# Performance work log

Hardware: AMD Instinct MI355X
Metric: run time of the kernel (lower is better)

The kernel has to match this reference:

```python
import jax, jax.numpy as jnp
import numpy as np

B, T = 64, 64
HUMAN, IN = 64, 8
HS, ES, K = 1024, 1024, 7
PSI_H, PSI_LR = 1024, 30

_PAR_SHAPES = [(HS, HS), (HS,), (IN, HS), (HS, HUMAN), (IN, HUMAN - IN)]
_PAR_SIZES = [int(np.prod(s)) for s in _PAR_SHAPES]
N_PSI = int(sum(_PAR_SIZES))
_OFFS = np.cumsum([0] + _PAR_SIZES)


def setup_inputs() -> dict:
    key = jax.random.key(0)
    ks = jax.random.split(key, 16)
    def xav(k, shape):
        lim = float(np.sqrt(6.0 / (shape[0] + shape[1])))
        return jax.random.uniform(k, shape, minval=-lim, maxval=lim, dtype=jnp.float32)
    def uni(k, shape, s):
        return jax.random.uniform(k, shape, minval=-s, maxval=s, dtype=jnp.float32)
    se = float(1.0 / np.sqrt(ES))
    return {
        "inputs": jax.random.normal(ks[0], (B, T, IN), jnp.float32),
        "outputs": jax.random.normal(ks[1], (B, T, HUMAN), jnp.float32),
        "eps": jax.random.normal(ks[2], (B, K), jnp.float32),
        "enc_Wih": uni(ks[3], (3 * ES, HUMAN), se),
        "enc_Whh": uni(ks[4], (3 * ES, ES), se),
        "enc_bih": uni(ks[5], (3 * ES,), se),
        "enc_bhh": uni(ks[6], (3 * ES,), se),
        "to_mu": xav(ks[7], (ES, K)),
        "to_lsigma": xav(ks[8], (ES, K)),
        "to_lsigma_bias": -0.5 * jnp.ones((K,), jnp.float32),
        "W1": xav(ks[9], (K, PSI_H)),
        "b1": jnp.zeros((PSI_H,), jnp.float32),
        "W2": xav(ks[10], (PSI_H, PSI_LR)),
        "b2": jnp.zeros((PSI_LR,), jnp.float32),
        "W3": xav(ks[11], (PSI_LR, N_PSI)),
        "b3": jnp.zeros((N_PSI,), jnp.float32),
        "gru_Wih": xav(ks[12], (IN, 2 * HS)),
        "gru_Whh": xav(ks[13], (HS, 2 * HS)),
        "gru_bias": jnp.concatenate([jnp.zeros((HS,)), jnp.ones((HS,))]).astype(jnp.float32),
    }


def _gru_cell(h, x, Wih, Whh, bih, bhh):
    # torch.nn.GRUCell math, gate order (r, z, n)
    gx = x @ Wih.T + bih
    gh = h @ Whh.T + bhh
    xr, xz, xn = jnp.split(gx, 3, axis=-1)
    hr, hz, hn = jnp.split(gh, 3, axis=-1)
    r = jax.nn.sigmoid(xr + hr)
    z = jax.nn.sigmoid(xz + hz)
    n = jnp.tanh(xn + r * hn)
    return (1.0 - z) * n + z * h


def _split_psi(psi):
    # psi: [B, N_PSI] -> per-sample (Whh, bh, Wih, C, D)
    return [psi[:, _OFFS[i]:_OFFS[i + 1]].reshape((-1,) + _PAR_SHAPES[i]) for i in range(5)]


def reference(inputs, outputs, eps, enc_Wih, enc_Whh, enc_bih, enc_bhh,
              to_mu, to_lsigma, to_lsigma_bias, W1, b1, W2, b2, W3, b3,
              gru_Wih, gru_Whh, gru_bias):
    bsz = inputs.shape[0]
    # ---- encoder: GRUCell over time-major outputs ----
    out_tm = jnp.swapaxes(outputs, 0, 1)  # [T, B, HUMAN]
    h0 = jnp.zeros((bsz, ES), inputs.dtype)
    h_enc = _gru_cell(h0, out_tm[0], enc_Wih, enc_Whh, enc_bih, enc_bhh)
    def enc_step(h, x):
        h = _gru_cell(h, x, enc_Wih, enc_Whh, enc_bih, enc_bhh)
        return h, None
    h_enc, _ = jax.lax.scan(enc_step, h_enc, out_tm[1:])
    mu = h_enc @ to_mu                       # [B, K]
    logstd = h_enc @ to_lsigma + to_lsigma_bias
    z = mu + eps * jnp.exp(logstd)
    # ---- hypernetwork psi decoder ----
    psi = (jnp.tanh(z @ W1 + b1) @ W2 + b2) @ W3 + b3   # [B, N_PSI]
    Whh_b, bh_b, Wih_b, C_b, D_b = _split_psi(psi)
    # ---- per-sample GRU decoder, vectorized over batch, scan over time ----
    gx_all = jnp.einsum('bti,ij->tbj', inputs, gru_Wih)  # [T, B, 2*HS]
    xW_all = jnp.einsum('bti,bih->tbh', inputs, Wih_b)   # [T, B, HS]

    def dec_step(h, xs):
        gx_t, xW_t = xs
        pre = gx_t + h @ gru_Whh + gru_bias   # [B, 2*HS]
        z_t = jax.nn.sigmoid(pre[:, :HS])
        r_t = jax.nn.sigmoid(pre[:, HS:])
        hWhh = jnp.einsum('bh,bhk->bk', h, Whh_b) + bh_b
        eta = jnp.tanh(xW_t + r_t * jnp.tanh(hWhh))
        h_new = z_t * h + (1.0 - z_t) * eta
        return h_new, h_new

    state0 = jnp.zeros((bsz, HS), inputs.dtype)
    h_last, dec_seq = jax.lax.scan(dec_step, state0, (gx_all, xW_all))
    dec_seq = jnp.swapaxes(dec_seq, 0, 1)    # [B, T, HS]
    # ---- readout ----
    yhats = jnp.einsum('bth,bhm->btm', dec_seq, C_b)
    xD = jnp.einsum('bti,bim->btm', inputs, D_b)  # [B, T, HUMAN-IN]
    yhats = yhats + jnp.concatenate([jnp.zeros_like(inputs), xD], axis=-1)
    # residual output
    yhats = yhats + jnp.concatenate(
        [inputs, jnp.zeros((bsz, inputs.shape[1], HUMAN - IN), inputs.dtype)], axis=-1)
    states = jax.lax.stop_gradient(h_last)
    return yhats, mu, logstd, states
```

## Files before the change

kernel.cpp:

```cpp
#include <hip/hip_runtime.h>

namespace {
constexpr int nT = 64;
constexpr int nK = 7;
constexpr long N_PSI = 1123776;
constexpr long SZ_WHH = 1048576;
constexpr long REST_SZ = 75200;
constexpr long R_BH = 0;
constexpr long R_WIH = 1024;
constexpr long R_C = 9216;
constexpr long R_D = 74752;
constexpr int NCH = 16;
constexpr int CHR = 64;
constexpr long PHALF = (long)NCH * 64 * 1024;
}

typedef __attribute__((ext_vector_type(4))) unsigned short us4;

__device__ __forceinline__ float b2f(unsigned short u) {
  return __uint_as_float(((unsigned int)u) << 16);
}
__device__ __forceinline__ unsigned short f2b(float f) {
  unsigned int u = __float_as_uint(f);
  return (unsigned short)((u + 0x7fffu + ((u >> 16) & 1u)) >> 16);
}
__device__ __forceinline__ float sigm(float x) { return 1.f / (1.f + __expf(-x)); }

__global__ void transpose_bf16_k(const float* __restrict__ in, unsigned short* __restrict__ out,
                                 int rows, int cols) {
  __shared__ float tile[32][33];
  int x = blockIdx.x * 32 + threadIdx.x;
  int y = blockIdx.y * 32 + threadIdx.y;
  #pragma unroll
  for (int i = 0; i < 32; i += 8)
    if ((y + i) < rows && x < cols) tile[threadIdx.y + i][threadIdx.x] = in[(long)(y + i) * cols + x];
  __syncthreads();
  x = blockIdx.y * 32 + threadIdx.x;
  y = blockIdx.x * 32 + threadIdx.y;
  #pragma unroll
  for (int i = 0; i < 32; i += 8)
    if ((y + i) < cols && x < rows) out[(long)(y + i) * rows + x] = f2b(tile[threadIdx.x][threadIdx.y + i]);
}

__global__ void cvt_bf16_k(const float* __restrict__ in, unsigned short* __restrict__ out, long n) {
  long i = (long)blockIdx.x * 256 + threadIdx.x;
  if (i < n) out[i] = f2b(in[i]);
}

__global__ __launch_bounds__(256) void enc_gx_k(const float* __restrict__ outputs,
                                                const unsigned short* __restrict__ WtWihB,
                                                const float* __restrict__ bih,
                                                unsigned short* __restrict__ gxE) {
  int g0 = blockIdx.x * 256;
  int btg = blockIdx.y;
  __shared__ unsigned short ws[64 * 256];
  __shared__ float xs[64][64];
  for (int i = threadIdx.x; i < 64 * 256; i += 256)
    ws[i] = WtWihB[(long)(i >> 8) * 3072 + g0 + (i & 255)];
  for (int i = threadIdx.x; i < 64 * 64; i += 256) {
    int idx = btg * 64 + (i >> 6);
    int t = idx >> 6, b = idx & 63;
    xs[i >> 6][i & 63] = outputs[((long)b * nT + t) * 64 + (i & 63)];
  }
  __syncthreads();
  float bihv = bih[g0 + threadIdx.x];
  for (int j = 0; j < 64; ++j) {
    int idx = btg * 64 + j;
    float acc = bihv;
    #pragma unroll 8
    for (int i = 0; i < 64; ++i) acc += xs[j][i] * b2f(ws[i * 256 + threadIdx.x]);
    gxE[(long)idx * 3072 + g0 + threadIdx.x] = f2b(acc);
  }
}

__global__ __launch_bounds__(256) void dec_gx_k(const float* __restrict__ inputs,
                                                const float* __restrict__ gWih,
                                                const float* __restrict__ gbias,
                                                unsigned short* __restrict__ gxD) {
  int g0 = blockIdx.x * 256;
  int btg = blockIdx.y;
  __shared__ float ws[8][256];
  __shared__ float xs[64][8];
  for (int i = threadIdx.x; i < 8 * 256; i += 256)
    ws[i >> 8][i & 255] = gWih[(long)(i >> 8) * 2048 + g0 + (i & 255)];
  for (int i = threadIdx.x; i < 64 * 8; i += 256) {
    int idx = btg * 64 + (i >> 3);
    int t = idx >> 6, b = idx & 63;
    xs[i >> 3][i & 7] = inputs[((long)b * nT + t) * 8 + (i & 7)];
  }
  __syncthreads();
  float bv = gbias[g0 + threadIdx.x];
  for (int j = 0; j < 64; ++j) {
    int idx = btg * 64 + j;
    float acc = bv;
    #pragma unroll
    for (int i = 0; i < 8; ++i) acc += xs[j][i] * ws[i][threadIdx.x];
    gxD[(long)idx * 2048 + g0 + threadIdx.x] = f2b(acc);
  }
}

__global__ __launch_bounds__(256) void xW_k(const float* __restrict__ inputs,
                                            const float* __restrict__ Rest,
                                            unsigned short* __restrict__ xWb) {
  int k0 = blockIdx.x * 256;
  int b = blockIdx.y;
  __shared__ float ws[8][256];
  __shared__ float xs[64][8];
  const float* RB = Rest + (long)b * REST_SZ + R_WIH;
  for (int i = threadIdx.x; i < 8 * 256; i += 256)
    ws[i >> 8][i & 255] = RB[(long)(i >> 8) * 1024 + k0 + (i & 255)];
  for (int i = threadIdx.x; i < 64 * 8; i += 256)
    xs[i >> 3][i & 7] = inputs[((long)b * nT + (i >> 3)) * 8 + (i & 7)];
  __syncthreads();
  for (int t = 0; t < 64; ++t) {
    float acc = 0.f;
    #pragma unroll
    for (int i = 0; i < 8; ++i) acc += xs[t][i] * ws[i][threadIdx.x];
    xWb[((long)t * 64 + b) * 1024 + k0 + threadIdx.x] = f2b(acc);
  }
}

__global__ __launch_bounds__(256) void enc_step_k(
    const unsigned short* __restrict__ W,
    const unsigned short* __restrict__ gxE,
    const float* __restrict__ bhh,
    float* __restrict__ hEnc,
    const float* __restrict__ pRr, const float* __restrict__ pZr, const float* __restrict__ pNr,
    float* __restrict__ pRw, float* __restrict__ pZw, float* __restrict__ pNw,
    int t) {
  int c = blockIdx.x & (NCH - 1);
  int sp = blockIdx.x >> 4;
  int b0 = sp * 2, b1 = b0 + 1;
  __shared__ float h0s[CHR], h1s[CHR];

  int v = threadIdx.x;
  if (v < 2 * CHR) {
    int hi = v >> 6;
    int bb = hi ? b1 : b0;
    int e = c * CHR + (v & 63);
    float sr = 0.f, sz = 0.f, sn = 0.f;
    if (t > 0) {
      #pragma unroll
      for (int cc = 0; cc < NCH; ++cc) {
        long base = ((long)cc * 64 + bb) * 1024 + e;
        sr += pRr[base]; sz += pZr[base]; sn += pNr[base];
      }
    }
    long gb = ((long)t * 64 + bb) * 3072;
    float xr = b2f(gxE[gb + e]), xz = b2f(gxE[gb + 1024 + e]), xn = b2f(gxE[gb + 2048 + e]);
    float hr = sr + bhh[e], hz = sz + bhh[1024 + e], hn = sn + bhh[2048 + e];
    float r = sigm(xr + hr);
    float z = sigm(xz + hz);
    float n = tanhf(xn + r * hn);
    float hold = 0.f;
    if (t > 0) hold = hEnc[(long)bb * 1024 + e];
    float hnew = (1.f - z) * n + z * hold;
    hEnc[(long)bb * 1024 + e] = hnew;
    if (hi) h1s[v & 63] = hnew; else h0s[v & 63] = hnew;
  }
  __syncthreads();

  if (t < nT - 1) {
    int e0 = threadIdx.x * 4;
    float ar0[4] = {}, az0[4] = {}, an0[4] = {}, ar1[4] = {}, az1[4] = {}, an1[4] = {};
    const unsigned short* Wb = W + (long)(c * CHR) * 3072 + e0;
    #pragma unroll 4
    for (int j = 0; j < CHR; ++j) {
      us4 wr = *(const us4*)(Wb + (long)j * 3072);
      us4 wz = *(const us4*)(Wb + (long)j * 3072 + 1024);
      us4 wn = *(const us4*)(Wb + (long)j * 3072 + 2048);
      float hv0 = h0s[j], hv1 = h1s[j];
      #pragma unroll
      for (int q = 0; q < 4; ++q) {
        float fr = b2f(wr[q]), fz = b2f(wz[q]), fn = b2f(wn[q]);
        ar0[q] += hv0 * fr; az0[q] += hv0 * fz; an0[q] += hv0 * fn;
        ar1[q] += hv1 * fr; az1[q] += hv1 * fz; an1[q] += hv1 * fn;
      }
    }
    long i0 = ((long)c * 64 + b0) * 1024 + e0;
    long i1 = i0 + 1024;
    *(float4*)(pRw + i0) = make_float4(ar0[0], ar0[1], ar0[2], ar0[3]);
    *(float4*)(pZw + i0) = make_float4(az0[0], az0[1], az0[2], az0[3]);
    *(float4*)(pNw + i0) = make_float4(an0[0], an0[1], an0[2], an0[3]);
    *(float4*)(pRw + i1) = make_float4(ar1[0], ar1[1], ar1[2], ar1[3]);
    *(float4*)(pZw + i1) = make_float4(az1[0], az1[1], az1[2], az1[3]);
    *(float4*)(pNw + i1) = make_float4(an1[0], an1[1], an1[2], an1[3]);
  }
}

__global__ void latent_k(const float* __restrict__ h_enc,
                         const float* __restrict__ to_mu, const float* __restrict__ to_lsig,
                         const float* __restrict__ lsig_bias, const float* __restrict__ eps,
                         float* __restrict__ out_mu, float* __restrict__ out_lsig,
                         float* __restrict__ zlat) {
  int b = blockIdx.x;
  __shared__ float hs[1024];
  for (int i = threadIdx.x; i < 1024; i += blockDim.x) hs[i] = h_enc[b * 1024 + i];
  __syncthreads();
  int k = threadIdx.x;
  if (k < nK) {
    float am = 0.f, as = 0.f;
    for (int h = 0; h < 1024; ++h) { float hv = hs[h]; am += hv * to_mu[h * nK + k]; as += hv * to_lsig[h * nK + k]; }
    float ls = as + lsig_bias[k];
    out_mu[b * nK + k] = am;
    out_lsig[b * nK + k] = ls;
    zlat[b * nK + k] = am + eps[b * nK + k] * __expf(ls);
  }
}

__global__ __launch_bounds__(256) void hyper_k(const float* __restrict__ zlat,
                                               const float* __restrict__ W1, const float* __restrict__ b1,
                                               const float* __restrict__ W2, const float* __restrict__ b2,
                                               float* __restrict__ a2out) {
  int b = blockIdx.x;
  __shared__ float a1[1024];
  __shared__ float zv[nK];
  if (threadIdx.x < nK) zv[threadIdx.x] = zlat[b * nK + threadIdx.x];
  __syncthreads();
  for (int j = threadIdx.x; j < 1024; j += 256) {
    float acc = b1[j];
    #pragma unroll
    for (int i = 0; i < nK; ++i) acc += zv[i] * W1[i * 1024 + j];
    a1[j] = tanhf(acc);
  }
  __syncthreads();
  int l = threadIdx.x >> 3;
  int s = threadIdx.x & 7;
  if (l < 30) {
    float acc = 0.f;
    for (int j = s; j < 1024; j += 8) acc += a1[j] * W2[j * 30 + l];
    acc += __shfl_xor(acc, 4);
    acc += __shfl_xor(acc, 2);
    acc += __shfl_xor(acc, 1);
    if (s == 0) a2out[b * 30 + l] = acc + b2[l];
  }
}

__global__ __launch_bounds__(256) void psi_k(const float* __restrict__ a2,
                                             const float* __restrict__ W3, const float* __restrict__ b3,
                                             unsigned short* __restrict__ WhhB, float* __restrict__ Rest) {
  __shared__ float sa[64 * 30];
  for (int i = threadIdx.x; i < 64 * 30; i += 256) sa[i] = a2[i];
  long n = (long)blockIdx.x * 256 + threadIdx.x;
  __syncthreads();
  if (n >= N_PSI) return;
  float w[30];
  #pragma unroll
  for (int l = 0; l < 30; ++l) w[l] = W3[(long)l * N_PSI + n];
  float bb = b3[n];
  bool isWhh = (n < SZ_WHH);
  for (int b = 0; b < 64; ++b) {
    float acc = bb;
    const float* ab = &sa[b * 30];
    #pragma unroll
    for (int l = 0; l < 30; ++l) acc += ab[l] * w[l];
    if (isWhh) WhhB[(long)b * SZ_WHH + n] = f2b(acc);
    else       Rest[(long)b * REST_SZ + (n - SZ_WHH)] = acc;
  }
}

__global__ __launch_bounds__(256) void dec_step_k(
    const unsigned short* __restrict__ WhhB,
    const unsigned short* __restrict__ gWhhB,
    const unsigned short* __restrict__ gxD,
    const unsigned short* __restrict__ xWb,
    const float* __restrict__ Rest,
    float* __restrict__ decS,
    const float* __restrict__ pZr, const float* __restrict__ pRr, const float* __restrict__ pWr,
    float* __restrict__ pZw, float* __restrict__ pRw, float* __restrict__ pWw,
    int t) {
  int c = blockIdx.x & (NCH - 1);
  int sp = blockIdx.x >> 4;
  int b0 = sp * 2, b1 = b0 + 1;
  __shared__ float h0s[CHR], h1s[CHR];

  int v = threadIdx.x;
  if (v < 2 * CHR) {
    int hi = v >> 6;
    int bb = hi ? b1 : b0;
    int k = c * CHR + (v & 63);
    float sz = 0.f, sr = 0.f, sw = 0.f;
    float hold = 0.f;
    if (t > 0) {
      #pragma unroll
      for (int cc = 0; cc < NCH; ++cc) {
        long base = ((long)cc * 64 + bb) * 1024 + k;
        sz += pZr[base]; sr += pRr[base]; sw += pWr[base];
      }
      hold = decS[((long)bb * nT + (t - 1)) * 1024 + k];
    }
    long gb = ((long)t * 64 + bb) * 2048;
    float gz = b2f(gxD[gb + k]), gr = b2f(gxD[gb + 1024 + k]);
    float z = sigm(gz + sz);
    float r = sigm(gr + sr);
    float hW = sw + Rest[(long)bb * REST_SZ + R_BH + k];
    float xw = b2f(xWb[((long)t * 64 + bb) * 1024 + k]);
    float eta = tanhf(xw + r * tanhf(hW));
    float hnew = z * hold + (1.f - z) * eta;
    decS[((long)bb * nT + t) * 1024 + k] = hnew;
    if (hi) h1s[v & 63] = hnew; else h0s[v & 63] = hnew;
  }
  __syncthreads();

  if (t < nT - 1) {
    int k0 = threadIdx.x * 4;
    float az0[4] = {}, ar0[4] = {}, aw0[4] = {}, az1[4] = {}, ar1[4] = {}, aw1[4] = {};
    const unsigned short* G = gWhhB + (long)(c * CHR) * 2048 + k0;
    const unsigned short* W0 = WhhB + (long)b0 * SZ_WHH + (long)(c * CHR) * 1024 + k0;
    const unsigned short* W1p = WhhB + (long)b1 * SZ_WHH + (long)(c * CHR) * 1024 + k0;
    #pragma unroll 4
    for (int j = 0; j < CHR; ++j) {
      us4 wz = *(const us4*)(G + (long)j * 2048);
      us4 wr = *(const us4*)(G + (long)j * 2048 + 1024);
      us4 w0 = *(const us4*)(W0 + (long)j * 1024);
      us4 w1 = *(const us4*)(W1p + (long)j * 1024);
      float hv0 = h0s[j], hv1 = h1s[j];
      #pragma unroll
      for (int q = 0; q < 4; ++q) {
        float fz = b2f(wz[q]), fr = b2f(wr[q]), f0 = b2f(w0[q]), f1 = b2f(w1[q]);
        az0[q] += hv0 * fz; ar0[q] += hv0 * fr; aw0[q] += hv0 * f0;
        az1[q] += hv1 * fz; ar1[q] += hv1 * fr; aw1[q] += hv1 * f1;
      }
    }
    long i0 = ((long)c * 64 + b0) * 1024 + k0;
    long i1 = i0 + 1024;
    *(float4*)(pZw + i0) = make_float4(az0[0], az0[1], az0[2], az0[3]);
    *(float4*)(pRw + i0) = make_float4(ar0[0], ar0[1], ar0[2], ar0[3]);
    *(float4*)(pWw + i0) = make_float4(aw0[0], aw0[1], aw0[2], aw0[3]);
    *(float4*)(pZw + i1) = make_float4(az1[0], az1[1], az1[2], az1[3]);
    *(float4*)(pRw + i1) = make_float4(ar1[0], ar1[1], ar1[2], ar1[3]);
    *(float4*)(pWw + i1) = make_float4(aw1[0], aw1[1], aw1[2], aw1[3]);
  }
}

__global__ __launch_bounds__(256) void readout_k(
    const float* __restrict__ dec_seq, const float* __restrict__ inputs,
    const float* __restrict__ Rest, float* __restrict__ yhats) {
  int b = blockIdx.x >> 3;
  int tg = blockIdx.x & 7;
  __shared__ float ss[8][1024];
  __shared__ float part[4][8][64];
  for (int i = threadIdx.x; i < 8 * 1024; i += 256)
    ss[i >> 10][i & 1023] = dec_seq[((long)b * nT + tg * 8 + (i >> 10)) * 1024 + (i & 1023)];
  __syncthreads();
  int m = threadIdx.x & 63, hq = threadIdx.x >> 6;
  const float* C = Rest + (long)b * REST_SZ + R_C;
  float acc[8] = {};
  for (int h = hq * 256; h < hq * 256 + 256; ++h) {
    float cv = C[(long)h * 64 + m];
    #pragma unroll
    for (int tt = 0; tt < 8; ++tt) acc[tt] += ss[tt][h] * cv;
  }
  #pragma unroll
  for (int tt = 0; tt < 8; ++tt) part[hq][tt][m] = acc[tt];
  __syncthreads();
  const float* D = Rest + (long)b * REST_SZ + R_D;
  for (int o = threadIdx.x; o < 512; o += 256) {
    int tt = o >> 6, mm = o & 63;
    float a = part[0][tt][mm] + part[1][tt][mm] + part[2][tt][mm] + part[3][tt][mm];
    long bt = (long)b * nT + tg * 8 + tt;
    if (mm < 8) {
      a += inputs[bt * 8 + mm];
    } else {
      #pragma unroll
      for (int i = 0; i < 8; ++i) a += inputs[bt * 8 + i] * D[i * 56 + (mm - 8)];
    }
    yhats[bt * 64 + mm] = a;
  }
}

__global__ void copy_states_k(const float* __restrict__ dec_seq, float* __restrict__ states) {
  int i = blockIdx.x * 256 + threadIdx.x;
  int b = i >> 10, h = i & 1023;
  states[i] = dec_seq[((long)b * nT + (nT - 1)) * 1024 + h];
}

extern "C" void kernel_launch(void* const* d_in, const int* in_sizes, int n_in,
                              void* d_out, int out_size, void* d_ws, size_t ws_size,
                              hipStream_t stream) {
  const float* inputs  = (const float*)d_in[0];
  const float* outputs = (const float*)d_in[1];
  const float* eps     = (const float*)d_in[2];
  const float* enc_Wih = (const float*)d_in[3];
  const float* enc_Whh = (const float*)d_in[4];
  const float* enc_bih = (const float*)d_in[5];
  const float* enc_bhh = (const float*)d_in[6];
  const float* to_mu   = (const float*)d_in[7];
  const float* to_lsig = (const float*)d_in[8];
  const float* lsig_b  = (const float*)d_in[9];
  const float* W1 = (const float*)d_in[10];
  const float* b1 = (const float*)d_in[11];
  const float* W2 = (const float*)d_in[12];
  const float* b2 = (const float*)d_in[13];
  const float* W3 = (const float*)d_in[14];
  const float* b3 = (const float*)d_in[15];
  const float* gWih  = (const float*)d_in[16];
  const float* gWhh  = (const float*)d_in[17];
  const float* gbias = (const float*)d_in[18];

  char* ws = (char*)d_ws;
  size_t off = 0;
  auto alloc = [&](size_t bytes) { size_t o = off; off = (off + bytes + 255) & ~(size_t)255; return o; };
  size_t oWhhB   = alloc(64ull * SZ_WHH * 2);
  size_t oRest   = alloc(64ull * REST_SZ * 4);
  size_t ogWhhB  = alloc(1024ull * 2048 * 2);
  size_t oWtWhhB = alloc(1024ull * 3072 * 2);
  size_t oWtWihB = alloc(64ull * 3072 * 2);
  size_t ogxE    = alloc(64ull * 64 * 3072 * 2);
  size_t ogxD    = alloc(64ull * 64 * 2048 * 2);
  size_t oxWb    = alloc(64ull * 64 * 1024 * 2);
  size_t opA     = alloc((size_t)2 * PHALF * 4);
  size_t opB     = alloc((size_t)2 * PHALF * 4);
  size_t opC     = alloc((size_t)2 * PHALF * 4);
  size_t ohA     = alloc(64ull * 1024 * 4);
  size_t oDec    = alloc(64ull * 64 * 1024 * 4);
  size_t oZ      = alloc(64 * nK * 4);
  size_t oA2     = alloc(64 * 30 * 4);
  (void)ws_size; (void)in_sizes; (void)n_in; (void)out_size;

  unsigned short* WhhB   = (unsigned short*)(ws + oWhhB);
  float*          Rest   = (float*)(ws + oRest);
  unsigned short* gWhhB  = (unsigned short*)(ws + ogWhhB);
  unsigned short* WtWhhB = (unsigned short*)(ws + oWtWhhB);
  unsigned short* WtWihB = (unsigned short*)(ws + oWtWihB);
  unsigned short* gxE    = (unsigned short*)(ws + ogxE);
  unsigned short* gxD    = (unsigned short*)(ws + ogxD);
  unsigned short* xWb    = (unsigned short*)(ws + oxWb);
  float* pA   = (float*)(ws + opA);
  float* pB   = (float*)(ws + opB);
  float* pC   = (float*)(ws + opC);
  float* hA   = (float*)(ws + ohA);
  float* decS = (float*)(ws + oDec);
  float* zlat = (float*)(ws + oZ);
  float* a2   = (float*)(ws + oA2);

  float* out    = (float*)d_out;
  float* out_yh = out;
  float* out_mu = out + 262144;
  float* out_ls = out + 262144 + 448;
  float* out_st = out + 262144 + 896;

  transpose_bf16_k<<<dim3(32, 96), dim3(32, 8), 0, stream>>>(enc_Whh, WtWhhB, 3072, 1024);
  transpose_bf16_k<<<dim3(2, 96),  dim3(32, 8), 0, stream>>>(enc_Wih, WtWihB, 3072, 64);
  cvt_bf16_k<<<(int)((1024ull * 2048 + 255) / 256), 256, 0, stream>>>(gWhh, gWhhB, 1024 * 2048);

  enc_gx_k<<<dim3(12, 64), 256, 0, stream>>>(outputs, WtWihB, enc_bih, gxE);

  for (int t = 0; t < nT; ++t) {
    int rp = t & 1, wp = (t + 1) & 1;
    enc_step_k<<<512, 256, 0, stream>>>(WtWhhB, gxE, enc_bhh, hA,
        pA + (size_t)rp * PHALF, pB + (size_t)rp * PHALF, pC + (size_t)rp * PHALF,
        pA + (size_t)wp * PHALF, pB + (size_t)wp * PHALF, pC + (size_t)wp * PHALF, t);
  }

  latent_k<<<64, 64, 0, stream>>>(hA, to_mu, to_lsig, lsig_b, eps, out_mu, out_ls, zlat);
  hyper_k<<<64, 256, 0, stream>>>(zlat, W1, b1, W2, b2, a2);
  psi_k<<<(int)((N_PSI + 255) / 256), 256, 0, stream>>>(a2, W3, b3, WhhB, Rest);

  dec_gx_k<<<dim3(8, 64), 256, 0, stream>>>(inputs, gWih, gbias, gxD);
  xW_k<<<dim3(4, 64), 256, 0, stream>>>(inputs, Rest, xWb);

  for (int t = 0; t < nT; ++t) {
    int rp = t & 1, wp = (t + 1) & 1;
    dec_step_k<<<512, 256, 0, stream>>>(WhhB, gWhhB, gxD, xWb, Rest, decS,
        pA + (size_t)rp * PHALF, pB + (size_t)rp * PHALF, pC + (size_t)rp * PHALF,
        pA + (size_t)wp * PHALF, pB + (size_t)wp * PHALF, pC + (size_t)wp * PHALF, t);
  }

  readout_k<<<512, 256, 0, stream>>>(decS, inputs, Rest, out_yh);
  copy_states_k<<<256, 256, 0, stream>>>(decS, out_st);
}
```

Baseline: 3.185 ms.

## Split recurrent steps into finer chunks, fuse latent/hyper kernels, vectorize psi

Encoder and decoder step kernels now split the hidden dimension into 32 chunks of 32 rows instead of 16 of 64, doubling the grid to 1024 blocks. The cross-chunk partial-sum reduction is spread across all 256 threads and finished through shared memory. The intent is more parallelism per sequential step and less time per block in the matvec. The cost is twice the partial-sum traffic and reduction work. Separately, latent_k and hyper_k are fused into one kernel with a warp-parallel latent dot product, and psi_k handles two outputs per thread with float2 and packed bf16 stores.

Result: slower. 3.401 ms (+6.8%).

```diff
diff --git a/kernel.cpp b/kernel.cpp
--- a/kernel.cpp
+++ b/kernel.cpp
@@ -10,12 +10,13 @@
 constexpr long R_WIH = 1024;
 constexpr long R_C = 9216;
 constexpr long R_D = 74752;
-constexpr int NCH = 16;
-constexpr int CHR = 64;
+constexpr int NCH = 32;
+constexpr int CHR = 32;
 constexpr long PHALF = (long)NCH * 64 * 1024;
 }
 
 typedef __attribute__((ext_vector_type(4))) unsigned short us4;
+typedef __attribute__((ext_vector_type(2))) unsigned short us2;
 
 __device__ __forceinline__ float b2f(unsigned short u) {
   return __uint_as_float(((unsigned int)u) << 16);
@@ -129,34 +130,45 @@
     float* __restrict__ pRw, float* __restrict__ pZw, float* __restrict__ pNw,
     int t) {
   int c = blockIdx.x & (NCH - 1);
-  int sp = blockIdx.x >> 4;
+  int sp = blockIdx.x >> 5;
   int b0 = sp * 2, b1 = b0 + 1;
   __shared__ float h0s[CHR], h1s[CHR];
+  __shared__ float redR[4][64], redZ[4][64], redN[4][64];
 
   int v = threadIdx.x;
-  if (v < 2 * CHR) {
-    int hi = v >> 6;
+  int q = v >> 6, idx = v & 63;
+  {
+    int hi = idx >> 5, e_in = idx & 31;
     int bb = hi ? b1 : b0;
-    int e = c * CHR + (v & 63);
+    int e = c * CHR + e_in;
     float sr = 0.f, sz = 0.f, sn = 0.f;
     if (t > 0) {
       #pragma unroll
-      for (int cc = 0; cc < NCH; ++cc) {
+      for (int cc = q * 8; cc < q * 8 + 8; ++cc) {
         long base = ((long)cc * 64 + bb) * 1024 + e;
         sr += pRr[base]; sz += pZr[base]; sn += pNr[base];
       }
     }
+    redR[q][idx] = sr; redZ[q][idx] = sz; redN[q][idx] = sn;
+  }
+  __syncthreads();
+  if (v < 64) {
+    int hi = v >> 5, e_in = v & 31;
+    int bb = hi ? b1 : b0;
+    int e = c * CHR + e_in;
+    float sr = redR[0][v] + redR[1][v] + redR[2][v] + redR[3][v];
+    float sz = redZ[0][v] + redZ[1][v] + redZ[2][v] + redZ[3][v];
+    float sn = redN[0][v] + redN[1][v] + redN[2][v] + redN[3][v];
     long gb = ((long)t * 64 + bb) * 3072;
     float xr = b2f(gxE[gb + e]), xz = b2f(gxE[gb + 1024 + e]), xn = b2f(gxE[gb + 2048 + e]);
     float hr = sr + bhh[e], hz = sz + bhh[1024 + e], hn = sn + bhh[2048 + e];
     float r = sigm(xr + hr);
     float z = sigm(xz + hz);
     float n = tanhf(xn + r * hn);
-    float hold = 0.f;
-    if (t > 0) hold = hEnc[(long)bb * 1024 + e];
+    float hold = (t > 0) ? hEnc[(long)bb * 1024 + e] : 0.f;
     float hnew = (1.f - z) * n + z * hold;
     hEnc[(long)bb * 1024 + e] = hnew;
-    if (hi) h1s[v & 63] = hnew; else h0s[v & 63] = hnew;
+    if (hi) h1s[e_in] = hnew; else h0s[e_in] = hnew;
   }
   __syncthreads();
 
@@ -171,10 +183,10 @@
       us4 wn = *(const us4*)(Wb + (long)j * 3072 + 2048);
       float hv0 = h0s[j], hv1 = h1s[j];
       #pragma unroll
-      for (int q = 0; q < 4; ++q) {
-        float fr = b2f(wr[q]), fz = b2f(wz[q]), fn = b2f(wn[q]);
-        ar0[q] += hv0 * fr; az0[q] += hv0 * fz; an0[q] += hv0 * fn;
-        ar1[q] += hv1 * fr; az1[q] += hv1 * fz; an1[q] += hv1 * fn;
+      for (int qq = 0; qq < 4; ++qq) {
+        float fr = b2f(wr[qq]), fz = b2f(wz[qq]), fn = b2f(wn[qq]);
+        ar0[qq] += hv0 * fr; az0[qq] += hv0 * fz; an0[qq] += hv0 * fn;
+        ar1[qq] += hv1 * fr; az1[qq] += hv1 * fz; an1[qq] += hv1 * fn;
       }
     }
     long i0 = ((long)c * 64 + b0) * 1024 + e0;
@@ -188,34 +200,37 @@
   }
 }
 
-__global__ void latent_k(const float* __restrict__ h_enc,
-                         const float* __restrict__ to_mu, const float* __restrict__ to_lsig,
-                         const float* __restrict__ lsig_bias, const float* __restrict__ eps,
-                         float* __restrict__ out_mu, float* __restrict__ out_lsig,
-                         float* __restrict__ zlat) {
+__global__ __launch_bounds__(256) void latent_hyper_k(
+    const float* __restrict__ h_enc,
+    const float* __restrict__ to_mu, const float* __restrict__ to_lsig,
+    const float* __restrict__ lsig_bias, const float* __restrict__ eps,
+    const float* __restrict__ W1, const float* __restrict__ b1,
+    const float* __restrict__ W2, const float* __restrict__ b2,
+    float* __restrict__ out_mu, float* __restrict__ out_lsig,
+    float* __restrict__ a2out) {
   int b = blockIdx.x;
   __shared__ float hs[1024];
-  for (int i = threadIdx.x; i < 1024; i += blockDim.x) hs[i] = h_enc[b * 1024 + i];
-  __syncthreads();
-  int k = threadIdx.x;
-  if (k < nK) {
-    float am = 0.f, as = 0.f;
-    for (int h = 0; h < 1024; ++h) { float hv = hs[h]; am += hv * to_mu[h * nK + k]; as += hv * to_lsig[h * nK + k]; }
-    float ls = as + lsig_bias[k];
-    out_mu[b * nK + k] = am;
-    out_lsig[b * nK + k] = ls;
-    zlat[b * nK + k] = am + eps[b * nK + k] * __expf(ls);
-  }
-}
-
-__global__ __launch_bounds__(256) void hyper_k(const float* __restrict__ zlat,
-                                               const float* __restrict__ W1, const float* __restrict__ b1,
-                                               const float* __restrict__ W2, const float* __restrict__ b2,
-                                               float* __restrict__ a2out) {
-  int b = blockIdx.x;
+  __shared__ float zv[8];
   __shared__ float a1[1024];
-  __shared__ float zv[nK];
-  if (threadIdx.x < nK) zv[threadIdx.x] = zlat[b * nK + threadIdx.x];
+  for (int i = threadIdx.x; i < 1024; i += 256) hs[i] = h_enc[b * 1024 + i];
+  __syncthreads();
+  int g = threadIdx.x >> 5, s = threadIdx.x & 31;
+  if (g < nK) {
+    float am = 0.f, as_ = 0.f;
+    for (int h = s; h < 1024; h += 32) {
+      float hv = hs[h];
+      am += hv * to_mu[h * nK + g];
+      as_ += hv * to_lsig[h * nK + g];
+    }
+    #pragma unroll
+    for (int m = 16; m >= 1; m >>= 1) { am += __shfl_xor(am, m); as_ += __shfl_xor(as_, m); }
+    if (s == 0) {
+      float ls = as_ + lsig_bias[g];
+      out_mu[b * nK + g] = am;
+      out_lsig[b * nK + g] = ls;
+      zv[g] = am + eps[b * nK + g] * __expf(ls);
+    }
+  }
   __syncthreads();
   for (int j = threadIdx.x; j < 1024; j += 256) {
     float acc = b1[j];
@@ -224,15 +239,14 @@
     a1[j] = tanhf(acc);
   }
   __syncthreads();
-  int l = threadIdx.x >> 3;
-  int s = threadIdx.x & 7;
+  int l = threadIdx.x >> 3, s8 = threadIdx.x & 7;
   if (l < 30) {
     float acc = 0.f;
-    for (int j = s; j < 1024; j += 8) acc += a1[j] * W2[j * 30 + l];
+    for (int j = s8; j < 1024; j += 8) acc += a1[j] * W2[j * 30 + l];
     acc += __shfl_xor(acc, 4);
     acc += __shfl_xor(acc, 2);
     acc += __shfl_xor(acc, 1);
-    if (s == 0) a2out[b * 30 + l] = acc + b2[l];
+    if (s8 == 0) a2out[b * 30 + l] = acc + b2[l];
   }
 }
 
@@ -241,21 +255,25 @@
                                              unsigned short* __restrict__ WhhB, float* __restrict__ Rest) {
   __shared__ float sa[64 * 30];
   for (int i = threadIdx.x; i < 64 * 30; i += 256) sa[i] = a2[i];
-  long n = (long)blockIdx.x * 256 + threadIdx.x;
-  __syncthreads();
-  if (n >= N_PSI) return;
-  float w[30];
+  long n0 = ((long)blockIdx.x * 256 + threadIdx.x) * 2;
+  __syncthreads();
+  if (n0 >= N_PSI) return;
+  float2 w[30];
   #pragma unroll
-  for (int l = 0; l < 30; ++l) w[l] = W3[(long)l * N_PSI + n];
-  float bb = b3[n];
-  bool isWhh = (n < SZ_WHH);
+  for (int l = 0; l < 30; ++l) w[l] = *(const float2*)(W3 + (long)l * N_PSI + n0);
+  float2 bb = *(const float2*)(b3 + n0);
+  bool isWhh = (n0 < SZ_WHH);
   for (int b = 0; b < 64; ++b) {
-    float acc = bb;
+    float a0 = bb.x, a1v = bb.y;
     const float* ab = &sa[b * 30];
     #pragma unroll
-    for (int l = 0; l < 30; ++l) acc += ab[l] * w[l];
-    if (isWhh) WhhB[(long)b * SZ_WHH + n] = f2b(acc);
-    else       Rest[(long)b * REST_SZ + (n - SZ_WHH)] = acc;
+    for (int l = 0; l < 30; ++l) { float av = ab[l]; a0 += av * w[l].x; a1v += av * w[l].y; }
+    if (isWhh) {
+      us2 o; o[0] = f2b(a0); o[1] = f2b(a1v);
+      *(us2*)(WhhB + (long)b * SZ_WHH + n0) = o;
+    } else {
+      *(float2*)(Rest + (long)b * REST_SZ + (n0 - SZ_WHH)) = make_float2(a0, a1v);
+    }
   }
 }
 
@@ -270,25 +288,35 @@
     float* __restrict__ pZw, float* __restrict__ pRw, float* __restrict__ pWw,
     int t) {
   int c = blockIdx.x & (NCH - 1);
-  int sp = blockIdx.x >> 4;
+  int sp = blockIdx.x >> 5;
   int b0 = sp * 2, b1 = b0 + 1;
   __shared__ float h0s[CHR], h1s[CHR];
+  __shared__ float redZ[4][64], redR[4][64], redW[4][64];
 
   int v = threadIdx.x;
-  if (v < 2 * CHR) {
-    int hi = v >> 6;
+  int q = v >> 6, idx = v & 63;
+  {
+    int hi = idx >> 5, e_in = idx & 31;
     int bb = hi ? b1 : b0;
-    int k = c * CHR + (v & 63);
+    int k = c * CHR + e_in;
     float sz = 0.f, sr = 0.f, sw = 0.f;
-    float hold = 0.f;
     if (t > 0) {
       #pragma unroll
-      for (int cc = 0; cc < NCH; ++cc) {
+      for (int cc = q * 8; cc < q * 8 + 8; ++cc) {
         long base = ((long)cc * 64 + bb) * 1024 + k;
         sz += pZr[base]; sr += pRr[base]; sw += pWr[base];
       }
-      hold = decS[((long)bb * nT + (t - 1)) * 1024 + k];
-    }
+    }
+    redZ[q][idx] = sz; redR[q][idx] = sr; redW[q][idx] = sw;
+  }
+  __syncthreads();
+  if (v < 64) {
+    int hi = v >> 5, e_in = v & 31;
+    int bb = hi ? b1 : b0;
+    int k = c * CHR + e_in;
+    float sz = redZ[0][v] + redZ[1][v] + redZ[2][v] + redZ[3][v];
+    float sr = redR[0][v] + redR[1][v] + redR[2][v] + redR[3][v];
+    float sw = redW[0][v] + redW[1][v] + redW[2][v] + redW[3][v];
     long gb = ((long)t * 64 + bb) * 2048;
     float gz = b2f(gxD[gb + k]), gr = b2f(gxD[gb + 1024 + k]);
     float z = sigm(gz + sz);
@@ -296,9 +324,10 @@
     float hW = sw + Rest[(long)bb * REST_SZ + R_BH + k];
     float xw = b2f(xWb[((long)t * 64 + bb) * 1024 + k]);
     float eta = tanhf(xw + r * tanhf(hW));
+    float hold = (t > 0) ? decS[((long)bb * nT + (t - 1)) * 1024 + k] : 0.f;
     float hnew = z * hold + (1.f - z) * eta;
     decS[((long)bb * nT + t) * 1024 + k] = hnew;
-    if (hi) h1s[v & 63] = hnew; else h0s[v & 63] = hnew;
+    if (hi) h1s[e_in] = hnew; else h0s[e_in] = hnew;
   }
   __syncthreads();
 
@@ -316,10 +345,10 @@
       us4 w1 = *(const us4*)(W1p + (long)j * 1024);
       float hv0 = h0s[j], hv1 = h1s[j];
       #pragma unroll
-      for (int q = 0; q < 4; ++q) {
-        float fz = b2f(wz[q]), fr = b2f(wr[q]), f0 = b2f(w0[q]), f1 = b2f(w1[q]);
-        az0[q] += hv0 * fz; ar0[q] += hv0 * fr; aw0[q] += hv0 * f0;
-        az1[q] += hv1 * fz; ar1[q] += hv1 * fr; aw1[q] += hv1 * f1;
+      for (int qq = 0; qq < 4; ++qq) {
+        float fz = b2f(wz[qq]), fr = b2f(wr[qq]), f0 = b2f(w0[qq]), f1 = b2f(w1[qq]);
+        az0[qq] += hv0 * fz; ar0[qq] += hv0 * fr; aw0[qq] += hv0 * f0;
+        az1[qq] += hv1 * fz; ar1[qq] += hv1 * fr; aw1[qq] += hv1 * f1;
       }
     }
     long i0 = ((long)c * 64 + b0) * 1024 + k0;
@@ -416,7 +445,7 @@
   size_t oDec    = alloc(64ull * 64 * 1024 * 4);
   size_t oZ      = alloc(64 * nK * 4);
   size_t oA2     = alloc(64 * 30 * 4);
-  (void)ws_size; (void)in_sizes; (void)n_in; (void)out_size;
+  (void)ws_size; (void)in_sizes; (void)n_in; (void)out_size; (void)oZ;
 
   unsigned short* WhhB   = (unsigned short*)(ws + oWhhB);
   float*          Rest   = (float*)(ws + oRest);
@@ -431,7 +460,6 @@
   float* pC   = (float*)(ws + opC);
   float* hA   = (float*)(ws + ohA);
   float* decS = (float*)(ws + oDec);
-  float* zlat = (float*)(ws + oZ);
   float* a2   = (float*)(ws + oA2);
 
   float* out    = (float*)d_out;
@@ -448,21 +476,21 @@
 
   for (int t = 0; t < nT; ++t) {
     int rp = t & 1, wp = (t + 1) & 1;
-    enc_step_k<<<512, 256, 0, stream>>>(WtWhhB, gxE, enc_bhh, hA,
+    enc_step_k<<<1024, 256, 0, stream>>>(WtWhhB, gxE, enc_bhh, hA,
         pA + (size_t)rp * PHALF, pB + (size_t)rp * PHALF, pC + (size_t)rp * PHALF,
         pA + (size_t)wp * PHALF, pB + (size_t)wp * PHALF, pC + (size_t)wp * PHALF, t);
   }
 
-  latent_k<<<64, 64, 0, stream>>>(hA, to_mu, to_lsig, lsig_b, eps, out_mu, out_ls, zlat);
-  hyper_k<<<64, 256, 0, stream>>>(zlat, W1, b1, W2, b2, a2);
-  psi_k<<<(int)((N_PSI + 255) / 256), 256, 0, stream>>>(a2, W3, b3, WhhB, Rest);
+  latent_hyper_k<<<64, 256, 0, stream>>>(hA, to_mu, to_lsig, lsig_b, eps,
+                                         W1, b1, W2, b2, out_mu, out_ls, a2);
+  psi_k<<<(int)((N_PSI / 2 + 255) / 256), 256, 0, stream>>>(a2, W3, b3, WhhB, Rest);
 
   dec_gx_k<<<dim3(8, 64), 256, 0, stream>>>(inputs, gWih, gbias, gxD);
   xW_k<<<dim3(4, 64), 256, 0, stream>>>(inputs, Rest, xWb);
 
   for (int t = 0; t < nT; ++t) {
     int rp = t & 1, wp = (t + 1) & 1;
-    dec_step_k<<<512, 256, 0, stream>>>(WhhB, gWhhB, gxD, xWb, Rest, decS,
+    dec_step_k<<<1024, 256, 0, stream>>>(WhhB, gWhhB, gxD, xWb, Rest, decS,
         pA + (size_t)rp * PHALF, pB + (size_t)rp * PHALF, pC + (size_t)rp * PHALF,
         pA + (size_t)wp * PHALF, pB + (size_t)wp * PHALF, pC + (size_t)wp * PHALF, t);
   }
```
